# Optimization experiments

Hardware: AMD Instinct MI355X
Metric: run time of the kernel (lower is better)

The kernel has to match this reference:

```python
import jax, jax.numpy as jnp
import numpy as np

B, F, D = 4096, 39, 128          # batch, num_fields, embed_dim
FIELD_DIM = 10000                # per-field vocab (uniform)
K_SPACE = [1, 256, 512]
M_SPACE = [1, 2, 4]
THRESHOLD = 500
NUM = F                          # prior_flag all ones -> num == field_len
# pairs (j, m) actually used by forward: (0,0) plus all (j>=1, m)
PAIRS = [(0, 0)] + [(j, m) for j in range(1, len(K_SPACE)) for m in range(len(M_SPACE))]

def _rows(j, m):
    return NUM * THRESHOLD if j == 0 else NUM * K_SPACE[j]

def setup_inputs() -> dict:
    key = jax.random.key(0)
    ks = jax.random.split(key, 2 + 2 * len(PAIRS))
    inp = {
        "x": jax.random.randint(ks[0], (B, F), 0, FIELD_DIM),
        "arch_prob": jax.random.uniform(ks[1], (F, len(K_SPACE) * len(M_SPACE)), dtype=jnp.float32),
    }
    for n, (j, m) in enumerate(PAIRS):
        rows = _rows(j, m)
        inp[f"cb_{j}_{m}"] = jax.random.normal(ks[2 + 2 * n], (rows, D), dtype=jnp.float32)
        inp[f"idx_{j}_{m}"] = jax.random.randint(ks[3 + 2 * n], (F * FIELD_DIM, M_SPACE[m]), 0, rows)
    return inp

def reference(x, arch_prob, cb_0_0, idx_0_0, cb_1_0, idx_1_0, cb_1_1, idx_1_1,
              cb_1_2, idx_1_2, cb_2_0, idx_2_0, cb_2_1, idx_2_1, cb_2_2, idx_2_2):
    cbs = {(0, 0): cb_0_0, (1, 0): cb_1_0, (1, 1): cb_1_1, (1, 2): cb_1_2,
           (2, 0): cb_2_0, (2, 1): cb_2_1, (2, 2): cb_2_2}
    idxs = {(0, 0): idx_0_0, (1, 0): idx_1_0, (1, 1): idx_1_1, (1, 2): idx_1_2,
            (2, 0): idx_2_0, (2, 1): idx_2_1, (2, 2): idx_2_2}
    offsets = (FIELD_DIM * jnp.arange(F)).astype(x.dtype)   # offsets_a
    xg = x + offsets[None, :]                               # (B, F) global feature ids
    nM = len(M_SPACE)
    emb = jnp.zeros((B, F, D), dtype=jnp.float32)
    for (j, m) in PAIRS:                                    # small fixed set of 7 codebooks
        Mn = M_SPACE[m]
        plen = D // Mn
        idx = idxs[(j, m)][xg]                              # (B, F, Mn) codeword ids
        # original gathers the full row then slices [i*plen:(i+1)*plen] for subvector i;
        # reshape the codebook to (rows, Mn, plen) and gather only the needed slice.
        cb = cbs[(j, m)].reshape(-1, Mn, plen)
        gathered = cb[idx, jnp.arange(Mn)[None, None, :], :]  # (B, F, Mn, plen)
        scale = arch_prob[:, j * nM + m]                    # (F,) per-field arch weight
        emb = emb + (scale[None, :, None, None] * gathered).reshape(B, F, D)
    return emb
```

## Files before the change

kernel.cpp:

```cpp
#include <hip/hip_runtime.h>

#define BB 4096
#define FF 39
#define DD 128
#define FIELD_DIM 10000

__global__ __launch_bounds__(256) void mixq_embed(
    const int* __restrict__ x,
    const float* __restrict__ arch_prob,
    const float* __restrict__ cb00, const int* __restrict__ i00,
    const float* __restrict__ cb10, const int* __restrict__ i10,
    const float* __restrict__ cb11, const int* __restrict__ i11,
    const float* __restrict__ cb12, const int* __restrict__ i12,
    const float* __restrict__ cb20, const int* __restrict__ i20,
    const float* __restrict__ cb21, const int* __restrict__ i21,
    const float* __restrict__ cb22, const int* __restrict__ i22,
    float* __restrict__ out)
{
    const int nwg  = gridDim.x;
    const int perx = nwg >> 3;
    const int blk  = blockIdx.x;
    const int xcd  = blk & 7;
    const int h    = xcd >> 2;
    const int wh   = (xcd & 3) * perx + (blk >> 3);

    const int t   = (int)threadIdx.x;
    const int sub = (t >> 4) & 1;
    const int li  = t & 15;
    const int ii  = wh * 16 + ((t >> 5) << 1) + sub;
    const int f   = ii >> 12;
    const int bb  = ii & (BB - 1);
    const int d0  = (h << 6) + (li << 2);

    const int xg = x[bb * FF + f] + f * FIELD_DIM;
    const float* ap = arch_prob + f * 9;

    const int k4 = (h << 1) + (li >> 3);

    int r00 = i00[xg];
    int r10 = i10[xg];
    int r11 = i11[(size_t)xg * 2 + h];
    int r12 = i12[(size_t)xg * 4 + k4];
    int r20 = i20[xg];
    int r21 = i21[(size_t)xg * 2 + h];
    int r22 = i22[(size_t)xg * 4 + k4];

    float4 acc = make_float4(0.f, 0.f, 0.f, 0.f);

#define GATHER_FMA(cb, r, col)                                                \
    do {                                                                      \
        float4 v = *reinterpret_cast<const float4*>((cb) + (size_t)(r) * DD + d0); \
        float s = ap[col];                                                    \
        acc.x += s * v.x; acc.y += s * v.y;                                   \
        acc.z += s * v.z; acc.w += s * v.w;                                   \
    } while (0)

    GATHER_FMA(cb00, r00, 0);
    GATHER_FMA(cb10, r10, 3);
    GATHER_FMA(cb11, r11, 4);
    GATHER_FMA(cb12, r12, 5);
    GATHER_FMA(cb20, r20, 6);
    GATHER_FMA(cb21, r21, 7);
    GATHER_FMA(cb22, r22, 8);
#undef GATHER_FMA

    float* dst = out + ((size_t)bb * FF + f) * DD + d0;
    __builtin_nontemporal_store(acc.x, dst + 0);
    __builtin_nontemporal_store(acc.y, dst + 1);
    __builtin_nontemporal_store(acc.z, dst + 2);
    __builtin_nontemporal_store(acc.w, dst + 3);
}

extern "C" void kernel_launch(void* const* d_in, const int* in_sizes, int n_in,
                              void* d_out, int out_size, void* d_ws, size_t ws_size,
                              hipStream_t stream) {
    const int*   x  = (const int*)d_in[0];
    const float* ap = (const float*)d_in[1];
    const float* cb00 = (const float*)d_in[2];
    const int*   i00  = (const int*)d_in[3];
    const float* cb10 = (const float*)d_in[4];
    const int*   i10  = (const int*)d_in[5];
    const float* cb11 = (const float*)d_in[6];
    const int*   i11  = (const int*)d_in[7];
    const float* cb12 = (const float*)d_in[8];
    const int*   i12  = (const int*)d_in[9];
    const float* cb20 = (const float*)d_in[10];
    const int*   i20  = (const int*)d_in[11];
    const float* cb21 = (const float*)d_in[12];
    const int*   i21  = (const int*)d_in[13];
    const float* cb22 = (const float*)d_in[14];
    const int*   i22  = (const int*)d_in[15];
    float* out = (float*)d_out;

    const long long total_threads = (long long)BB * FF * 32;
    const int threads = 256;
    const int blocks = (int)((total_threads + threads - 1) / threads);

    mixq_embed<<<blocks, threads, 0, stream>>>(
        x, ap, cb00, i00, cb10, i10, cb11, i11, cb12, i12,
        cb20, i20, cb21, i21, cb22, i22, out);
}
```

Baseline: 88.06 us.

## Split into index-resolve pass and codebook-gather pass via packed workspace

Adds a first kernel that resolves all seven codeword indices per (batch, field) item with vectorized loads and packs them as 16-bit values into per-slice uint4 records in the workspace. A second kernel then gathers codebook slices using one 16-byte record load per thread, spreading each item across eight 16-column slices. The aim is to stop many threads from issuing redundant scattered index-table loads. In exchange it writes and re-reads an extra workspace buffer, adds a second launch, and relies on codebook row counts fitting in 16 bits (the largest is 19500). It falls back to the old kernel when the workspace is too small.

```diff
diff --git a/kernel.cpp b/kernel.cpp
--- a/kernel.cpp
+++ b/kernel.cpp
@@ -4,6 +4,110 @@
 #define FF 39
 #define DD 128
 #define FIELD_DIM 10000
+#define NITEMS (BB * FF)
+#define ROWS_WS_BYTES ((size_t)8 * NITEMS * 16)
+
+__global__ __launch_bounds__(256) void pass1_resolve(
+    const int* __restrict__ x,
+    const int* __restrict__ i00, const int* __restrict__ i10,
+    const int* __restrict__ i11, const int* __restrict__ i12,
+    const int* __restrict__ i20, const int* __restrict__ i21,
+    const int* __restrict__ i22,
+    uint4* __restrict__ rows_ws)
+{
+    const int nwg = gridDim.x;
+    const int cpx = nwg >> 3;
+    const int blk = blockIdx.x;
+    const int wg  = (blk & 7) * cpx + (blk >> 3);
+    const int i   = wg * 256 + (int)threadIdx.x;
+    const int f   = i >> 12;
+    const int b   = i & (BB - 1);
+    const int xg  = x[b * FF + f] + f * FIELD_DIM;
+
+    const unsigned r00 = (unsigned)i00[xg];
+    const unsigned r10 = (unsigned)i10[xg];
+    const unsigned r20 = (unsigned)i20[xg];
+    const int2 v11 = *reinterpret_cast<const int2*>(i11 + (size_t)xg * 2);
+    const int2 v21 = *reinterpret_cast<const int2*>(i21 + (size_t)xg * 2);
+    const int4 v12 = *reinterpret_cast<const int4*>(i12 + (size_t)xg * 4);
+    const int4 v22 = *reinterpret_cast<const int4*>(i22 + (size_t)xg * 4);
+
+    const unsigned r11_0 = (unsigned)v11.x, r11_1 = (unsigned)v11.y;
+    const unsigned r21_0 = (unsigned)v21.x, r21_1 = (unsigned)v21.y;
+    const unsigned r12_0 = (unsigned)v12.x, r12_1 = (unsigned)v12.y;
+    const unsigned r12_2 = (unsigned)v12.z, r12_3 = (unsigned)v12.w;
+    const unsigned r22_0 = (unsigned)v22.x, r22_1 = (unsigned)v22.y;
+    const unsigned r22_2 = (unsigned)v22.z, r22_3 = (unsigned)v22.w;
+
+    const unsigned w0 = r00 | (r10 << 16);
+
+#define EMIT(h, a, b4)                                                        \
+    do {                                                                      \
+        uint4 rec;                                                            \
+        rec.x = w0;                                                           \
+        rec.y = r20 | (r11_##a << 16);                                        \
+        rec.z = r21_##a | (r12_##b4 << 16);                                   \
+        rec.w = r22_##b4;                                                     \
+        rows_ws[(size_t)(h) * NITEMS + i] = rec;                              \
+    } while (0)
+
+    EMIT(0, 0, 0); EMIT(1, 0, 0); EMIT(2, 0, 1); EMIT(3, 0, 1);
+    EMIT(4, 1, 2); EMIT(5, 1, 2); EMIT(6, 1, 3); EMIT(7, 1, 3);
+#undef EMIT
+}
+
+__global__ __launch_bounds__(256) void pass2_gather(
+    const float* __restrict__ arch_prob,
+    const float* __restrict__ cb00, const float* __restrict__ cb10,
+    const float* __restrict__ cb11, const float* __restrict__ cb12,
+    const float* __restrict__ cb20, const float* __restrict__ cb21,
+    const float* __restrict__ cb22,
+    const uint4* __restrict__ rows_ws,
+    float* __restrict__ out)
+{
+    const int blk  = blockIdx.x;
+    const int h    = blk & 7;
+    const int seq  = blk >> 3;
+    const int t    = (int)threadIdx.x;
+    const int item = seq * 64 + (t >> 2);
+    const int sub  = t & 3;
+    const int d0   = h * 16 + sub * 4;
+    const int f    = item >> 12;
+    const int b    = item & (BB - 1);
+
+    const uint4 rw = rows_ws[(size_t)h * NITEMS + item];
+    const int r00 = (int)(rw.x & 0xffffu), r10 = (int)(rw.x >> 16);
+    const int r20 = (int)(rw.y & 0xffffu), r11 = (int)(rw.y >> 16);
+    const int r21 = (int)(rw.z & 0xffffu), r12 = (int)(rw.z >> 16);
+    const int r22 = (int)(rw.w & 0xffffu);
+
+    const float* ap = arch_prob + f * 9;
+
+    float4 acc = make_float4(0.f, 0.f, 0.f, 0.f);
+
+#define GATHER_FMA(cb, r, col)                                                \
+    do {                                                                      \
+        float4 v = *reinterpret_cast<const float4*>((cb) + (size_t)(r) * DD + d0); \
+        float s = ap[col];                                                    \
+        acc.x += s * v.x; acc.y += s * v.y;                                   \
+        acc.z += s * v.z; acc.w += s * v.w;                                   \
+    } while (0)
+
+    GATHER_FMA(cb00, r00, 0);
+    GATHER_FMA(cb10, r10, 3);
+    GATHER_FMA(cb11, r11, 4);
+    GATHER_FMA(cb12, r12, 5);
+    GATHER_FMA(cb20, r20, 6);
+    GATHER_FMA(cb21, r21, 7);
+    GATHER_FMA(cb22, r22, 8);
+#undef GATHER_FMA
+
+    float* dst = out + ((size_t)b * FF + f) * DD + d0;
+    __builtin_nontemporal_store(acc.x, dst + 0);
+    __builtin_nontemporal_store(acc.y, dst + 1);
+    __builtin_nontemporal_store(acc.z, dst + 2);
+    __builtin_nontemporal_store(acc.w, dst + 3);
+}
 
 __global__ __launch_bounds__(256) void mixq_embed(
     const int* __restrict__ x,
@@ -21,7 +125,7 @@
     const int perx = nwg >> 3;
     const int blk  = blockIdx.x;
     const int xcd  = blk & 7;
-    const int h    = xcd >> 2;
+    const int hh   = xcd >> 2;
     const int wh   = (xcd & 3) * perx + (blk >> 3);
 
     const int t   = (int)threadIdx.x;
@@ -30,19 +134,18 @@
     const int ii  = wh * 16 + ((t >> 5) << 1) + sub;
     const int f   = ii >> 12;
     const int bb  = ii & (BB - 1);
-    const int d0  = (h << 6) + (li << 2);
+    const int d0  = (hh << 6) + (li << 2);
 
     const int xg = x[bb * FF + f] + f * FIELD_DIM;
     const float* ap = arch_prob + f * 9;
-
-    const int k4 = (h << 1) + (li >> 3);
+    const int k4 = (hh << 1) + (li >> 3);
 
     int r00 = i00[xg];
     int r10 = i10[xg];
-    int r11 = i11[(size_t)xg * 2 + h];
+    int r11 = i11[(size_t)xg * 2 + hh];
     int r12 = i12[(size_t)xg * 4 + k4];
     int r20 = i20[xg];
-    int r21 = i21[(size_t)xg * 2 + h];
+    int r21 = i21[(size_t)xg * 2 + hh];
     int r22 = i22[(size_t)xg * 4 + k4];
 
     float4 acc = make_float4(0.f, 0.f, 0.f, 0.f);
@@ -92,11 +195,17 @@
     const int*   i22  = (const int*)d_in[15];
     float* out = (float*)d_out;
 
-    const long long total_threads = (long long)BB * FF * 32;
-    const int threads = 256;
-    const int blocks = (int)((total_threads + threads - 1) / threads);
-
-    mixq_embed<<<blocks, threads, 0, stream>>>(
-        x, ap, cb00, i00, cb10, i10, cb11, i11, cb12, i12,
-        cb20, i20, cb21, i21, cb22, i22, out);
-}
+    if (ws_size >= ROWS_WS_BYTES) {
+        uint4* rows_ws = (uint4*)d_ws;
+        pass1_resolve<<<NITEMS / 256, 256, 0, stream>>>(
+            x, i00, i10, i11, i12, i20, i21, i22, rows_ws);
+        pass2_gather<<<(NITEMS / 64) * 8, 256, 0, stream>>>(
+            ap, cb00, cb10, cb11, cb12, cb20, cb21, cb22, rows_ws, out);
+    } else {
+        const long long total_threads = (long long)BB * FF * 32;
+        const int blocks = (int)((total_threads + 255) / 256);
+        mixq_embed<<<blocks, 256, 0, stream>>>(
+            x, ap, cb00, i00, cb10, i10, cb11, i11, cb12, i12,
+            cb20, i20, cb21, i21, cb22, i22, out);
+    }
+}
```

Measured after the change: 133.9 us. 52.1% more time.
